# Performance work log

Measured on AMD Instinct MI355X. Metric: run time of the kernel, lower is better.

## Reference

```python
import jax, jax.numpy as jnp
import numpy as np


def setup_inputs() -> dict:
    key = jax.random.key(0)
    k1, k2 = jax.random.split(key)
    B, N, M = 16, 4096, 4096
    points1 = jax.random.normal(k1, (B, N, 3), dtype=jnp.float32)
    points2 = jax.random.normal(k2, (B, M, 3), dtype=jnp.float32)
    return {"points1": points1, "points2": points2}


def reference(points1, points2):
    # Mathematically equal to sum((x - y)^2) without materializing (B,N,M,3).
    w1 = 1.0
    w2 = 1.0
    sq1 = jnp.sum(points1 * points1, axis=-1)  # (B, N)
    sq2 = jnp.sum(points2 * points2, axis=-1)  # (B, M)
    cross = jnp.einsum("bnd,bmd->bnm", points1, points2)  # (B, N, M)
    dist = sq1[:, :, None] + sq2[:, None, :] - 2.0 * cross  # (B, N, M)
    dist_min1 = jnp.min(dist, axis=2)  # nearest in points2 for each point1
    dist_min2 = jnp.min(dist, axis=1)  # nearest in points1 for each point2
    B = points1.shape[0]
    return (w1 * jnp.sum(dist_min1) + w2 * jnp.sum(dist_min2)) / B
```

## Files before the change

### kernel.cpp

```cpp
#include <hip/hip_runtime.h>

typedef _Float16 half8 __attribute__((ext_vector_type(8)));
typedef float f32x16 __attribute__((ext_vector_type(16)));

#define NPTS   4096
#define BATCH  16
#define BLOCK  256
#define CHUNK  2048
#define NCHUNK 2
#define NBLK   512

__global__ __launch_bounds__(BLOCK, 2) void chamfer_mfma_kernel(
    const float* __restrict__ p1, const float* __restrict__ p2,
    float* __restrict__ partial)
{
    __shared__ half8 REC[CHUNK];

    const int tid  = threadIdx.x;
    const int lane = tid & 63;
    const int n    = lane & 31;
    const int grp  = lane >> 5;
    const int wv   = tid >> 6;
    const int blk  = blockIdx.x;
    const int j    = blk & 15;
    const int b    = (blk >> 4) & 15;
    const int dir  = blk >> 8;

    const float* selfp  = (dir == 0 ? p1 : p2) + (size_t)b * NPTS * 3;
    const float* otherp = (dir == 0 ? p2 : p1) + (size_t)b * NPTS * 3;

    const int base = j * 256 + wv * 64;
    half8 a0, a1;
    float ssq01;
    {
        const int i0 = (base + n) * 3, i1 = (base + 32 + n) * 3;
        float x0 = selfp[i0], y0 = selfp[i0 + 1], z0 = selfp[i0 + 2];
        float x1 = selfp[i1], y1 = selfp[i1 + 1], z1 = selfp[i1 + 2];
        ssq01 = fmaf(x0, x0, fmaf(y0, y0, z0 * z0)) +
                fmaf(x1, x1, fmaf(y1, y1, z1 * z1));
        _Float16 hx0 = (_Float16)x0, hy0 = (_Float16)y0, hz0 = (_Float16)z0;
        _Float16 lx0 = (_Float16)(x0 - (float)hx0);
        _Float16 ly0 = (_Float16)(y0 - (float)hy0);
        _Float16 lz0 = (_Float16)(z0 - (float)hz0);
        _Float16 hx1 = (_Float16)x1, hy1 = (_Float16)y1, hz1 = (_Float16)z1;
        _Float16 lx1 = (_Float16)(x1 - (float)hx1);
        _Float16 ly1 = (_Float16)(y1 - (float)hy1);
        _Float16 lz1 = (_Float16)(z1 - (float)hz1);
        const _Float16 c0 = (_Float16)0.f, c1 = (_Float16)1.f;
        if (grp == 0) {
            a0[0]=hx0; a0[1]=hy0; a0[2]=hz0; a0[3]=c0; a0[4]=c0; a0[5]=c0; a0[6]=c1; a0[7]=c0;
            a1[0]=hx1; a1[1]=hy1; a1[2]=hz1; a1[3]=c0; a1[4]=c0; a1[5]=c0; a1[6]=c1; a1[7]=c0;
        } else {
            a0[0]=lx0; a0[1]=ly0; a0[2]=lz0; a0[3]=hx0; a0[4]=hy0; a0[5]=hz0; a0[6]=c0; a0[7]=c1;
            a1[0]=lx1; a1[1]=ly1; a1[2]=lz1; a1[3]=hx1; a1[4]=hy1; a1[5]=hz1; a1[6]=c0; a1[7]=c1;
        }
    }

    f32x16 m0, m1, zc;
#pragma unroll
    for (int r = 0; r < 16; ++r) { m0[r] = 3.4e38f; m1[r] = 3.4e38f; zc[r] = 0.f; }

    for (int c = 0; c < NCHUNK; ++c) {
        __syncthreads();
        {
            const float4* src = (const float4*)(otherp + (size_t)c * CHUNK * 3);
            float4 v0 = src[tid * 6 + 0], v1 = src[tid * 6 + 1];
            float4 v2 = src[tid * 6 + 2], v3 = src[tid * 6 + 3];
            float4 v4 = src[tid * 6 + 4], v5 = src[tid * 6 + 5];
            float ox[8] = {v0.x, v0.w, v1.z, v2.y, v3.x, v3.w, v4.z, v5.y};
            float oy[8] = {v0.y, v1.x, v1.w, v2.z, v3.y, v4.x, v4.w, v5.z};
            float oz[8] = {v0.z, v1.y, v2.x, v2.w, v3.z, v4.y, v5.x, v5.w};
#pragma unroll
            for (int k = 0; k < 8; ++k) {
                float gx = -2.f * ox[k], gy = -2.f * oy[k], gz = -2.f * oz[k];
                float q  = fmaf(ox[k], ox[k], fmaf(oy[k], oy[k], oz[k] * oz[k]));
                _Float16 ghx = (_Float16)gx, ghy = (_Float16)gy, ghz = (_Float16)gz;
                half8 r;
                r[0] = ghx; r[1] = ghy; r[2] = ghz;
                r[3] = (_Float16)(gx - (float)ghx);
                r[4] = (_Float16)(gy - (float)ghy);
                r[5] = (_Float16)(gz - (float)ghz);
                _Float16 qh = (_Float16)q;
                r[6] = qh;
                r[7] = (_Float16)(q - (float)qh);
                REC[tid * 8 + k] = r;
            }
        }
        __syncthreads();
        const half8* rp = REC + n;
#pragma unroll 2
        for (int g = 0; g < 32; ++g) {
            half8 b0 = rp[g * 64];
            half8 b1 = rp[g * 64 + 32];
            f32x16 o00 = __builtin_amdgcn_mfma_f32_32x32x16_f16(a0, b0, zc, 0, 0, 0);
            f32x16 o01 = __builtin_amdgcn_mfma_f32_32x32x16_f16(a0, b1, zc, 0, 0, 0);
            f32x16 o10 = __builtin_amdgcn_mfma_f32_32x32x16_f16(a1, b0, zc, 0, 0, 0);
            f32x16 o11 = __builtin_amdgcn_mfma_f32_32x32x16_f16(a1, b1, zc, 0, 0, 0);
#pragma unroll
            for (int r = 0; r < 16; ++r) {
                m0[r] = fminf(fminf(o00[r], o01[r]), m0[r]);
                m1[r] = fminf(fminf(o10[r], o11[r]), m1[r]);
            }
        }
    }

#pragma unroll
    for (int mask = 1; mask <= 16; mask <<= 1) {
#pragma unroll
        for (int r = 0; r < 16; ++r) {
            m0[r] = fminf(m0[r], __shfl_xor((float)m0[r], mask, 64));
            m1[r] = fminf(m1[r], __shfl_xor((float)m1[r], mask, 64));
        }
    }
    float rowsum = 0.f;
#pragma unroll
    for (int r = 0; r < 16; ++r) rowsum += m0[r] + m1[r];
    rowsum += __shfl_xor(rowsum, 32, 64);

    float sv = grp ? 0.f : ssq01;
#pragma unroll
    for (int mask = 1; mask <= 16; mask <<= 1) sv += __shfl_xor(sv, mask, 64);

    if (lane == 0) partial[blk * 4 + wv] = rowsum + sv;
}

__global__ __launch_bounds__(256) void chamfer_reduce(
    const float* __restrict__ partial, float* __restrict__ out)
{
    float s = 0.f;
    for (int i = threadIdx.x; i < NBLK * 4; i += 256) s += partial[i];
#pragma unroll
    for (int off = 32; off > 0; off >>= 1) s += __shfl_down(s, off, 64);
    __shared__ float ws4[4];
    int lane = threadIdx.x & 63, wv = threadIdx.x >> 6;
    if (lane == 0) ws4[wv] = s;
    __syncthreads();
    if (threadIdx.x == 0)
        out[0] = (ws4[0] + ws4[1] + ws4[2] + ws4[3]) * (1.0f / BATCH);
}

extern "C" void kernel_launch(void* const* d_in, const int* in_sizes, int n_in,
                              void* d_out, int out_size, void* d_ws, size_t ws_size,
                              hipStream_t stream) {
    const float* p1 = (const float*)d_in[0];
    const float* p2 = (const float*)d_in[1];
    float* out = (float*)d_out;
    float* partial = (float*)d_ws;

    chamfer_mfma_kernel<<<dim3(NBLK), dim3(BLOCK), 0, stream>>>(p1, p2, partial);
    chamfer_reduce<<<dim3(1), dim3(256), 0, stream>>>(partial, out);
}
```

Measured before the change: 78.57 us.

## Split other-point chunk across wave pairs and merge mins through shared memory

Each block now covers 128 self points instead of 256, so the grid doubles to 1024 blocks. The four waves form two self-point groups, and within each group the two waves take different halves of the staged other-point chunk. The two halves' partial minima are combined through shared memory before the shuffle reduction. The aim is more parallelism and occupancy on the 256-CU MI355X (launch bounds raised to 4 blocks per SM). The cost is that each block loads and converts all other points for only half as many self points, doubling the global load and fp16 packing work, plus an extra LDS exchange and sync.

```diff
diff --git a/kernel.cpp b/kernel.cpp
--- a/kernel.cpp
+++ b/kernel.cpp
@@ -8,9 +8,9 @@
 #define BLOCK  256
 #define CHUNK  2048
 #define NCHUNK 2
-#define NBLK   512
+#define NBLK   1024
 
-__global__ __launch_bounds__(BLOCK, 2) void chamfer_mfma_kernel(
+__global__ __launch_bounds__(BLOCK, 4) void chamfer_mfma_kernel(
     const float* __restrict__ p1, const float* __restrict__ p2,
     float* __restrict__ partial)
 {
@@ -21,15 +21,17 @@
     const int n    = lane & 31;
     const int grp  = lane >> 5;
     const int wv   = tid >> 6;
+    const int sg   = wv & 1;
+    const int oh   = wv >> 1;
     const int blk  = blockIdx.x;
-    const int j    = blk & 15;
-    const int b    = (blk >> 4) & 15;
-    const int dir  = blk >> 8;
+    const int j    = blk & 31;
+    const int b    = (blk >> 5) & 15;
+    const int dir  = blk >> 9;
 
     const float* selfp  = (dir == 0 ? p1 : p2) + (size_t)b * NPTS * 3;
     const float* otherp = (dir == 0 ? p2 : p1) + (size_t)b * NPTS * 3;
 
-    const int base = j * 256 + wv * 64;
+    const int base = j * 128 + sg * 64;
     half8 a0, a1;
     float ssq01;
     {
@@ -87,9 +89,9 @@
             }
         }
         __syncthreads();
-        const half8* rp = REC + n;
+        const half8* rp = REC + oh * (CHUNK / 2) + n;
 #pragma unroll 2
-        for (int g = 0; g < 32; ++g) {
+        for (int g = 0; g < CHUNK / 2 / 64; ++g) {
             half8 b0 = rp[g * 64];
             half8 b1 = rp[g * 64 + 32];
             f32x16 o00 = __builtin_amdgcn_mfma_f32_32x32x16_f16(a0, b0, zc, 0, 0, 0);
@@ -104,31 +106,49 @@
         }
     }
 
-#pragma unroll
-    for (int mask = 1; mask <= 16; mask <<= 1) {
+    __syncthreads();
+    float* CW = (float*)REC;
+    if (oh == 1) {
 #pragma unroll
         for (int r = 0; r < 16; ++r) {
-            m0[r] = fminf(m0[r], __shfl_xor((float)m0[r], mask, 64));
-            m1[r] = fminf(m1[r], __shfl_xor((float)m1[r], mask, 64));
+            CW[((sg * 2 + 0) * 64 + lane) * 17 + r] = m0[r];
+            CW[((sg * 2 + 1) * 64 + lane) * 17 + r] = m1[r];
         }
     }
-    float rowsum = 0.f;
+    __syncthreads();
+    if (oh == 0) {
 #pragma unroll
-    for (int r = 0; r < 16; ++r) rowsum += m0[r] + m1[r];
-    rowsum += __shfl_xor(rowsum, 32, 64);
+        for (int r = 0; r < 16; ++r) {
+            m0[r] = fminf(m0[r], CW[((sg * 2 + 0) * 64 + lane) * 17 + r]);
+            m1[r] = fminf(m1[r], CW[((sg * 2 + 1) * 64 + lane) * 17 + r]);
+        }
+#pragma unroll
+        for (int mask = 1; mask <= 16; mask <<= 1) {
+#pragma unroll
+            for (int r = 0; r < 16; ++r) {
+                m0[r] = fminf(m0[r], __shfl_xor((float)m0[r], mask, 64));
+                m1[r] = fminf(m1[r], __shfl_xor((float)m1[r], mask, 64));
+            }
+        }
+        float rowsum = 0.f;
+#pragma unroll
+        for (int r = 0; r < 16; ++r) rowsum += m0[r] + m1[r];
+        rowsum += __shfl_xor(rowsum, 32, 64);
 
-    float sv = grp ? 0.f : ssq01;
+        float sv = grp ? 0.f : ssq01;
 #pragma unroll
-    for (int mask = 1; mask <= 16; mask <<= 1) sv += __shfl_xor(sv, mask, 64);
+        for (int mask = 1; mask <= 16; mask <<= 1)
+            sv += __shfl_xor(sv, mask, 64);
 
-    if (lane == 0) partial[blk * 4 + wv] = rowsum + sv;
+        if (lane == 0) partial[blk * 2 + sg] = rowsum + sv;
+    }
 }
 
 __global__ __launch_bounds__(256) void chamfer_reduce(
     const float* __restrict__ partial, float* __restrict__ out)
 {
     float s = 0.f;
-    for (int i = threadIdx.x; i < NBLK * 4; i += 256) s += partial[i];
+    for (int i = threadIdx.x; i < NBLK * 2; i += 256) s += partial[i];
 #pragma unroll
     for (int off = 32; off > 0; off >>= 1) s += __shfl_down(s, off, 64);
     __shared__ float ws4[4];
```

After: 81.99 us. 4.4% more time.

## Split other-point range across two wave groups with single full LDS stage

Applied to the files above, without the earlier changes.

Doubles the block to 512 threads so each of the four self-point wave slots gets two waves, each scanning half of the other cloud. The whole other cloud (4096 records) is staged into LDS once, removing the two-chunk loop and its extra barriers. The two halves' partial minima are merged through shared memory before the usual shuffle reduction. LDS use doubles to 64KB per block, which may cut blocks per CU, and the cross-wave merge adds a barrier and LDS traffic.

```diff
diff --git a/kernel.cpp b/kernel.cpp
--- a/kernel.cpp
+++ b/kernel.cpp
@@ -5,12 +5,11 @@
 
 #define NPTS   4096
 #define BATCH  16
-#define BLOCK  256
-#define CHUNK  2048
-#define NCHUNK 2
+#define BLOCK  512
+#define CHUNK  4096
 #define NBLK   512
 
-__global__ __launch_bounds__(BLOCK, 2) void chamfer_mfma_kernel(
+__global__ __launch_bounds__(BLOCK, 4) void chamfer_mfma_kernel(
     const float* __restrict__ p1, const float* __restrict__ p2,
     float* __restrict__ partial)
 {
@@ -21,6 +20,8 @@
     const int n    = lane & 31;
     const int grp  = lane >> 5;
     const int wv   = tid >> 6;
+    const int sg   = wv & 3;
+    const int oh   = wv >> 2;
     const int blk  = blockIdx.x;
     const int j    = blk & 15;
     const int b    = (blk >> 4) & 15;
@@ -29,7 +30,7 @@
     const float* selfp  = (dir == 0 ? p1 : p2) + (size_t)b * NPTS * 3;
     const float* otherp = (dir == 0 ? p2 : p1) + (size_t)b * NPTS * 3;
 
-    const int base = j * 256 + wv * 64;
+    const int base = j * 256 + sg * 64;
     half8 a0, a1;
     float ssq01;
     {
@@ -39,89 +40,100 @@
         ssq01 = fmaf(x0, x0, fmaf(y0, y0, z0 * z0)) +
                 fmaf(x1, x1, fmaf(y1, y1, z1 * z1));
         _Float16 hx0 = (_Float16)x0, hy0 = (_Float16)y0, hz0 = (_Float16)z0;
-        _Float16 lx0 = (_Float16)(x0 - (float)hx0);
-        _Float16 ly0 = (_Float16)(y0 - (float)hy0);
-        _Float16 lz0 = (_Float16)(z0 - (float)hz0);
         _Float16 hx1 = (_Float16)x1, hy1 = (_Float16)y1, hz1 = (_Float16)z1;
-        _Float16 lx1 = (_Float16)(x1 - (float)hx1);
-        _Float16 ly1 = (_Float16)(y1 - (float)hy1);
-        _Float16 lz1 = (_Float16)(z1 - (float)hz1);
         const _Float16 c0 = (_Float16)0.f, c1 = (_Float16)1.f;
         if (grp == 0) {
             a0[0]=hx0; a0[1]=hy0; a0[2]=hz0; a0[3]=c0; a0[4]=c0; a0[5]=c0; a0[6]=c1; a0[7]=c0;
             a1[0]=hx1; a1[1]=hy1; a1[2]=hz1; a1[3]=c0; a1[4]=c0; a1[5]=c0; a1[6]=c1; a1[7]=c0;
         } else {
-            a0[0]=lx0; a0[1]=ly0; a0[2]=lz0; a0[3]=hx0; a0[4]=hy0; a0[5]=hz0; a0[6]=c0; a0[7]=c1;
-            a1[0]=lx1; a1[1]=ly1; a1[2]=lz1; a1[3]=hx1; a1[4]=hy1; a1[5]=hz1; a1[6]=c0; a1[7]=c1;
+            a0[0]=(_Float16)(x0-(float)hx0); a0[1]=(_Float16)(y0-(float)hy0);
+            a0[2]=(_Float16)(z0-(float)hz0); a0[3]=hx0; a0[4]=hy0; a0[5]=hz0;
+            a0[6]=c0; a0[7]=c1;
+            a1[0]=(_Float16)(x1-(float)hx1); a1[1]=(_Float16)(y1-(float)hy1);
+            a1[2]=(_Float16)(z1-(float)hz1); a1[3]=hx1; a1[4]=hy1; a1[5]=hz1;
+            a1[6]=c0; a1[7]=c1;
         }
     }
+
+    {
+        const float4* src = (const float4*)otherp;
+        float4 v0 = src[tid * 6 + 0], v1 = src[tid * 6 + 1];
+        float4 v2 = src[tid * 6 + 2], v3 = src[tid * 6 + 3];
+        float4 v4 = src[tid * 6 + 4], v5 = src[tid * 6 + 5];
+        float ox[8] = {v0.x, v0.w, v1.z, v2.y, v3.x, v3.w, v4.z, v5.y};
+        float oy[8] = {v0.y, v1.x, v1.w, v2.z, v3.y, v4.x, v4.w, v5.z};
+        float oz[8] = {v0.z, v1.y, v2.x, v2.w, v3.z, v4.y, v5.x, v5.w};
+#pragma unroll
+        for (int k = 0; k < 8; ++k) {
+            float gx = -2.f * ox[k], gy = -2.f * oy[k], gz = -2.f * oz[k];
+            float q  = fmaf(ox[k], ox[k], fmaf(oy[k], oy[k], oz[k] * oz[k]));
+            _Float16 ghx = (_Float16)gx, ghy = (_Float16)gy, ghz = (_Float16)gz;
+            half8 r;
+            r[0] = ghx; r[1] = ghy; r[2] = ghz;
+            r[3] = (_Float16)(gx - (float)ghx);
+            r[4] = (_Float16)(gy - (float)ghy);
+            r[5] = (_Float16)(gz - (float)ghz);
+            _Float16 qh = (_Float16)q;
+            r[6] = qh;
+            r[7] = (_Float16)(q - (float)qh);
+            REC[tid * 8 + k] = r;
+        }
+    }
+    __syncthreads();
 
     f32x16 m0, m1, zc;
 #pragma unroll
     for (int r = 0; r < 16; ++r) { m0[r] = 3.4e38f; m1[r] = 3.4e38f; zc[r] = 0.f; }
 
-    for (int c = 0; c < NCHUNK; ++c) {
-        __syncthreads();
-        {
-            const float4* src = (const float4*)(otherp + (size_t)c * CHUNK * 3);
-            float4 v0 = src[tid * 6 + 0], v1 = src[tid * 6 + 1];
-            float4 v2 = src[tid * 6 + 2], v3 = src[tid * 6 + 3];
-            float4 v4 = src[tid * 6 + 4], v5 = src[tid * 6 + 5];
-            float ox[8] = {v0.x, v0.w, v1.z, v2.y, v3.x, v3.w, v4.z, v5.y};
-            float oy[8] = {v0.y, v1.x, v1.w, v2.z, v3.y, v4.x, v4.w, v5.z};
-            float oz[8] = {v0.z, v1.y, v2.x, v2.w, v3.z, v4.y, v5.x, v5.w};
+    const half8* rp = REC + oh * 2048 + n;
+#pragma unroll 2
+    for (int g = 0; g < 64; ++g) {
+        half8 bf = rp[g * 32];
+        f32x16 o0 = __builtin_amdgcn_mfma_f32_32x32x16_f16(a0, bf, zc, 0, 0, 0);
+        f32x16 o1 = __builtin_amdgcn_mfma_f32_32x32x16_f16(a1, bf, zc, 0, 0, 0);
 #pragma unroll
-            for (int k = 0; k < 8; ++k) {
-                float gx = -2.f * ox[k], gy = -2.f * oy[k], gz = -2.f * oz[k];
-                float q  = fmaf(ox[k], ox[k], fmaf(oy[k], oy[k], oz[k] * oz[k]));
-                _Float16 ghx = (_Float16)gx, ghy = (_Float16)gy, ghz = (_Float16)gz;
-                half8 r;
-                r[0] = ghx; r[1] = ghy; r[2] = ghz;
-                r[3] = (_Float16)(gx - (float)ghx);
-                r[4] = (_Float16)(gy - (float)ghy);
-                r[5] = (_Float16)(gz - (float)ghz);
-                _Float16 qh = (_Float16)q;
-                r[6] = qh;
-                r[7] = (_Float16)(q - (float)qh);
-                REC[tid * 8 + k] = r;
-            }
-        }
-        __syncthreads();
-        const half8* rp = REC + n;
-#pragma unroll 2
-        for (int g = 0; g < 32; ++g) {
-            half8 b0 = rp[g * 64];
-            half8 b1 = rp[g * 64 + 32];
-            f32x16 o00 = __builtin_amdgcn_mfma_f32_32x32x16_f16(a0, b0, zc, 0, 0, 0);
-            f32x16 o01 = __builtin_amdgcn_mfma_f32_32x32x16_f16(a0, b1, zc, 0, 0, 0);
-            f32x16 o10 = __builtin_amdgcn_mfma_f32_32x32x16_f16(a1, b0, zc, 0, 0, 0);
-            f32x16 o11 = __builtin_amdgcn_mfma_f32_32x32x16_f16(a1, b1, zc, 0, 0, 0);
-#pragma unroll
-            for (int r = 0; r < 16; ++r) {
-                m0[r] = fminf(fminf(o00[r], o01[r]), m0[r]);
-                m1[r] = fminf(fminf(o10[r], o11[r]), m1[r]);
-            }
+        for (int r = 0; r < 16; ++r) {
+            m0[r] = fminf(m0[r], o0[r]);
+            m1[r] = fminf(m1[r], o1[r]);
         }
     }
 
-#pragma unroll
-    for (int mask = 1; mask <= 16; mask <<= 1) {
+    __syncthreads();
+    float* CW = (float*)REC;
+    if (oh == 1) {
 #pragma unroll
         for (int r = 0; r < 16; ++r) {
-            m0[r] = fminf(m0[r], __shfl_xor((float)m0[r], mask, 64));
-            m1[r] = fminf(m1[r], __shfl_xor((float)m1[r], mask, 64));
+            CW[(sg * 64 + lane) * 33 + r]      = m0[r];
+            CW[(sg * 64 + lane) * 33 + 16 + r] = m1[r];
         }
     }
-    float rowsum = 0.f;
+    __syncthreads();
+    if (oh == 0) {
 #pragma unroll
-    for (int r = 0; r < 16; ++r) rowsum += m0[r] + m1[r];
-    rowsum += __shfl_xor(rowsum, 32, 64);
+        for (int r = 0; r < 16; ++r) {
+            m0[r] = fminf(m0[r], CW[(sg * 64 + lane) * 33 + r]);
+            m1[r] = fminf(m1[r], CW[(sg * 64 + lane) * 33 + 16 + r]);
+        }
+#pragma unroll
+        for (int mask = 1; mask <= 16; mask <<= 1) {
+#pragma unroll
+            for (int r = 0; r < 16; ++r) {
+                m0[r] = fminf(m0[r], __shfl_xor((float)m0[r], mask, 64));
+                m1[r] = fminf(m1[r], __shfl_xor((float)m1[r], mask, 64));
+            }
+        }
+        float rowsum = 0.f;
+#pragma unroll
+        for (int r = 0; r < 16; ++r) rowsum += m0[r] + m1[r];
+        rowsum += __shfl_xor(rowsum, 32, 64);
 
-    float sv = grp ? 0.f : ssq01;
+        float sv = grp ? 0.f : ssq01;
 #pragma unroll
-    for (int mask = 1; mask <= 16; mask <<= 1) sv += __shfl_xor(sv, mask, 64);
+        for (int mask = 1; mask <= 16; mask <<= 1)
+            sv += __shfl_xor(sv, mask, 64);
 
-    if (lane == 0) partial[blk * 4 + wv] = rowsum + sv;
+        if (lane == 0) partial[blk * 4 + sg] = rowsum + sv;
+    }
 }
 
 __global__ __launch_bounds__(256) void chamfer_reduce(
```

After: 79.63 us. About the same (+1.4%).

## Precompute split-fp16 records in a prep kernel and stream them from global memory

Applied to the files above, without the earlier changes.

A new prep kernel converts every point once into its hi/lo fp16 record (scaled by -2, with the split squared norm) and writes it to workspace, reducing the squared norms into per-block sums. The main kernel no longer builds records in shared memory per block. It reads them straight from global/L2 and drops the shared memory and both syncthreads. Each wave now covers 32 query rows instead of 64, the grid doubles to 1024 blocks, and occupancy is raised to 4 blocks per CU. The trade is an extra kernel launch, a workspace round trip, and half the MFMA reuse per B-fragment load.

```diff
diff --git a/kernel.cpp b/kernel.cpp
--- a/kernel.cpp
+++ b/kernel.cpp
@@ -5,130 +5,115 @@
 
 #define NPTS   4096
 #define BATCH  16
-#define BLOCK  256
-#define CHUNK  2048
-#define NCHUNK 2
-#define NBLK   512
+#define NREC   (2 * BATCH * NPTS)
+#define NPRE   512
+#define NMAIN  1024
+#define NPART  (NMAIN * 4)
 
-__global__ __launch_bounds__(BLOCK, 2) void chamfer_mfma_kernel(
+
+__global__ __launch_bounds__(256) void chamfer_prep(
     const float* __restrict__ p1, const float* __restrict__ p2,
-    float* __restrict__ partial)
+    half8* __restrict__ rec, float* __restrict__ qsum)
 {
-    __shared__ half8 REC[CHUNK];
+    const int gid = blockIdx.x * 256 + threadIdx.x;
+    const int dir = gid >> 16;
+    const int rem = gid & 0xFFFF;
+    const float* src = (dir == 0 ? p2 : p1) + (size_t)rem * 3;
+    float ox = src[0], oy = src[1], oz = src[2];
+    float gx = -2.f * ox, gy = -2.f * oy, gz = -2.f * oz;
+    float q  = fmaf(ox, ox, fmaf(oy, oy, oz * oz));
+    _Float16 ghx = (_Float16)gx, ghy = (_Float16)gy, ghz = (_Float16)gz;
+    half8 r;
+    r[0] = ghx; r[1] = ghy; r[2] = ghz;
+    r[3] = (_Float16)(gx - (float)ghx);
+    r[4] = (_Float16)(gy - (float)ghy);
+    r[5] = (_Float16)(gz - (float)ghz);
+    _Float16 qh = (_Float16)q;
+    r[6] = qh;
+    r[7] = (_Float16)(q - (float)qh);
+    rec[gid] = r;
 
+    float s = q;
+#pragma unroll
+    for (int off = 32; off > 0; off >>= 1) s += __shfl_down(s, off, 64);
+    __shared__ float ws4[4];
+    int lane = threadIdx.x & 63, wv = threadIdx.x >> 6;
+    if (lane == 0) ws4[wv] = s;
+    __syncthreads();
+    if (threadIdx.x == 0)
+        qsum[blockIdx.x] = ws4[0] + ws4[1] + ws4[2] + ws4[3];
+}
+
+__global__ __launch_bounds__(256, 4) void chamfer_main(
+    const float* __restrict__ p1, const float* __restrict__ p2,
+    const half8* __restrict__ rec, float* __restrict__ partial)
+{
     const int tid  = threadIdx.x;
     const int lane = tid & 63;
     const int n    = lane & 31;
     const int grp  = lane >> 5;
     const int wv   = tid >> 6;
     const int blk  = blockIdx.x;
-    const int j    = blk & 15;
-    const int b    = (blk >> 4) & 15;
-    const int dir  = blk >> 8;
+    const int j    = blk & 31;
+    const int b    = (blk >> 5) & 15;
+    const int dir  = blk >> 9;
 
-    const float* selfp  = (dir == 0 ? p1 : p2) + (size_t)b * NPTS * 3;
-    const float* otherp = (dir == 0 ? p2 : p1) + (size_t)b * NPTS * 3;
+    const float* selfp = (dir == 0 ? p1 : p2) + (size_t)b * NPTS * 3;
 
-    const int base = j * 256 + wv * 64;
-    half8 a0, a1;
-    float ssq01;
+    half8 a0;
     {
-        const int i0 = (base + n) * 3, i1 = (base + 32 + n) * 3;
-        float x0 = selfp[i0], y0 = selfp[i0 + 1], z0 = selfp[i0 + 2];
-        float x1 = selfp[i1], y1 = selfp[i1 + 1], z1 = selfp[i1 + 2];
-        ssq01 = fmaf(x0, x0, fmaf(y0, y0, z0 * z0)) +
-                fmaf(x1, x1, fmaf(y1, y1, z1 * z1));
-        _Float16 hx0 = (_Float16)x0, hy0 = (_Float16)y0, hz0 = (_Float16)z0;
-        _Float16 lx0 = (_Float16)(x0 - (float)hx0);
-        _Float16 ly0 = (_Float16)(y0 - (float)hy0);
-        _Float16 lz0 = (_Float16)(z0 - (float)hz0);
-        _Float16 hx1 = (_Float16)x1, hy1 = (_Float16)y1, hz1 = (_Float16)z1;
-        _Float16 lx1 = (_Float16)(x1 - (float)hx1);
-        _Float16 ly1 = (_Float16)(y1 - (float)hy1);
-        _Float16 lz1 = (_Float16)(z1 - (float)hz1);
+        const int i0 = (j * 128 + wv * 32 + n) * 3;
+        float x = selfp[i0], y = selfp[i0 + 1], z = selfp[i0 + 2];
+        _Float16 hx = (_Float16)x, hy = (_Float16)y, hz = (_Float16)z;
         const _Float16 c0 = (_Float16)0.f, c1 = (_Float16)1.f;
         if (grp == 0) {
-            a0[0]=hx0; a0[1]=hy0; a0[2]=hz0; a0[3]=c0; a0[4]=c0; a0[5]=c0; a0[6]=c1; a0[7]=c0;
-            a1[0]=hx1; a1[1]=hy1; a1[2]=hz1; a1[3]=c0; a1[4]=c0; a1[5]=c0; a1[6]=c1; a1[7]=c0;
+            a0[0] = hx; a0[1] = hy; a0[2] = hz;
+            a0[3] = c0; a0[4] = c0; a0[5] = c0; a0[6] = c1; a0[7] = c0;
         } else {
-            a0[0]=lx0; a0[1]=ly0; a0[2]=lz0; a0[3]=hx0; a0[4]=hy0; a0[5]=hz0; a0[6]=c0; a0[7]=c1;
-            a1[0]=lx1; a1[1]=ly1; a1[2]=lz1; a1[3]=hx1; a1[4]=hy1; a1[5]=hz1; a1[6]=c0; a1[7]=c1;
+            a0[0] = (_Float16)(x - (float)hx);
+            a0[1] = (_Float16)(y - (float)hy);
+            a0[2] = (_Float16)(z - (float)hz);
+            a0[3] = hx; a0[4] = hy; a0[5] = hz; a0[6] = c0; a0[7] = c1;
         }
     }
 
-    f32x16 m0, m1, zc;
+    f32x16 m, zc;
 #pragma unroll
-    for (int r = 0; r < 16; ++r) { m0[r] = 3.4e38f; m1[r] = 3.4e38f; zc[r] = 0.f; }
+    for (int r = 0; r < 16; ++r) { m[r] = 3.4e38f; zc[r] = 0.f; }
 
-    for (int c = 0; c < NCHUNK; ++c) {
-        __syncthreads();
-        {
-            const float4* src = (const float4*)(otherp + (size_t)c * CHUNK * 3);
-            float4 v0 = src[tid * 6 + 0], v1 = src[tid * 6 + 1];
-            float4 v2 = src[tid * 6 + 2], v3 = src[tid * 6 + 3];
-            float4 v4 = src[tid * 6 + 4], v5 = src[tid * 6 + 5];
-            float ox[8] = {v0.x, v0.w, v1.z, v2.y, v3.x, v3.w, v4.z, v5.y};
-            float oy[8] = {v0.y, v1.x, v1.w, v2.z, v3.y, v4.x, v4.w, v5.z};
-            float oz[8] = {v0.z, v1.y, v2.x, v2.w, v3.z, v4.y, v5.x, v5.w};
+    const half8* rp = rec + ((size_t)(dir * BATCH + b) << 12) + n;
+#pragma unroll 4
+    for (int g = 0; g < 64; ++g) {
+        half8 b0 = rp[(2 * g + 0) * 32];
+        half8 b1 = rp[(2 * g + 1) * 32];
+        f32x16 o0 = __builtin_amdgcn_mfma_f32_32x32x16_f16(a0, b0, zc, 0, 0, 0);
+        f32x16 o1 = __builtin_amdgcn_mfma_f32_32x32x16_f16(a0, b1, zc, 0, 0, 0);
 #pragma unroll
-            for (int k = 0; k < 8; ++k) {
-                float gx = -2.f * ox[k], gy = -2.f * oy[k], gz = -2.f * oz[k];
-                float q  = fmaf(ox[k], ox[k], fmaf(oy[k], oy[k], oz[k] * oz[k]));
-                _Float16 ghx = (_Float16)gx, ghy = (_Float16)gy, ghz = (_Float16)gz;
-                half8 r;
-                r[0] = ghx; r[1] = ghy; r[2] = ghz;
-                r[3] = (_Float16)(gx - (float)ghx);
-                r[4] = (_Float16)(gy - (float)ghy);
-                r[5] = (_Float16)(gz - (float)ghz);
-                _Float16 qh = (_Float16)q;
-                r[6] = qh;
-                r[7] = (_Float16)(q - (float)qh);
-                REC[tid * 8 + k] = r;
-            }
-        }
-        __syncthreads();
-        const half8* rp = REC + n;
-#pragma unroll 2
-        for (int g = 0; g < 32; ++g) {
-            half8 b0 = rp[g * 64];
-            half8 b1 = rp[g * 64 + 32];
-            f32x16 o00 = __builtin_amdgcn_mfma_f32_32x32x16_f16(a0, b0, zc, 0, 0, 0);
-            f32x16 o01 = __builtin_amdgcn_mfma_f32_32x32x16_f16(a0, b1, zc, 0, 0, 0);
-            f32x16 o10 = __builtin_amdgcn_mfma_f32_32x32x16_f16(a1, b0, zc, 0, 0, 0);
-            f32x16 o11 = __builtin_amdgcn_mfma_f32_32x32x16_f16(a1, b1, zc, 0, 0, 0);
-#pragma unroll
-            for (int r = 0; r < 16; ++r) {
-                m0[r] = fminf(fminf(o00[r], o01[r]), m0[r]);
-                m1[r] = fminf(fminf(o10[r], o11[r]), m1[r]);
-            }
-        }
+        for (int r = 0; r < 16; ++r)
+            m[r] = fminf(fminf(o0[r], o1[r]), m[r]);
     }
 
 #pragma unroll
     for (int mask = 1; mask <= 16; mask <<= 1) {
 #pragma unroll
-        for (int r = 0; r < 16; ++r) {
-            m0[r] = fminf(m0[r], __shfl_xor((float)m0[r], mask, 64));
-            m1[r] = fminf(m1[r], __shfl_xor((float)m1[r], mask, 64));
-        }
+        for (int r = 0; r < 16; ++r)
+            m[r] = fminf(m[r], __shfl_xor((float)m[r], mask, 64));
     }
     float rowsum = 0.f;
 #pragma unroll
-    for (int r = 0; r < 16; ++r) rowsum += m0[r] + m1[r];
+    for (int r = 0; r < 16; ++r) rowsum += m[r];
     rowsum += __shfl_xor(rowsum, 32, 64);
 
-    float sv = grp ? 0.f : ssq01;
-#pragma unroll
-    for (int mask = 1; mask <= 16; mask <<= 1) sv += __shfl_xor(sv, mask, 64);
-
-    if (lane == 0) partial[blk * 4 + wv] = rowsum + sv;
+    if (lane == 0) partial[blk * 4 + wv] = rowsum;
 }
 
 __global__ __launch_bounds__(256) void chamfer_reduce(
-    const float* __restrict__ partial, float* __restrict__ out)
+    const float* __restrict__ partial, const float* __restrict__ qsum,
+    float* __restrict__ out)
 {
     float s = 0.f;
-    for (int i = threadIdx.x; i < NBLK * 4; i += 256) s += partial[i];
+    for (int i = threadIdx.x; i < NPART; i += 256) s += partial[i];
+    for (int i = threadIdx.x; i < NPRE; i += 256) s += qsum[i];
 #pragma unroll
     for (int off = 32; off > 0; off >>= 1) s += __shfl_down(s, off, 64);
     __shared__ float ws4[4];
@@ -145,8 +130,11 @@
     const float* p1 = (const float*)d_in[0];
     const float* p2 = (const float*)d_in[1];
     float* out = (float*)d_out;
-    float* partial = (float*)d_ws;
+    half8* rec     = (half8*)d_ws;
+    float* partial = (float*)((char*)d_ws + (size_t)NREC * 16);
+    float* qsum    = partial + NPART;
 
-    chamfer_mfma_kernel<<<dim3(NBLK), dim3(BLOCK), 0, stream>>>(p1, p2, partial);
-    chamfer_reduce<<<dim3(1), dim3(256), 0, stream>>>(partial, out);
+    chamfer_prep<<<dim3(NPRE), dim3(256), 0, stream>>>(p1, p2, rec, qsum);
+    chamfer_main<<<dim3(NMAIN), dim3(256), 0, stream>>>(p1, p2, rec, partial);
+    chamfer_reduce<<<dim3(1), dim3(256), 0, stream>>>(partial, qsum, out);
 }
```

Result: slower. 87.31 us (+11.1%).
